# Kernel tuning notes

Hardware: AMD Instinct MI355X
Metric: run time of the kernel (lower is better)

The kernel has to match this reference:

```python
import jax, jax.numpy as jnp
import numpy as np

S, HID, H, D, G = 2048, 4096, 32, 128, 2   # seq, hidden, heads, head_dim, kv groups
ROT = D // 2                               # rotary applied to first half of head_dim
QKV = HID + 2 * G * D                      # 4608


def setup_inputs() -> dict:
    key = jax.random.key(0)
    k1, k2, k3 = jax.random.split(key, 3)
    sc = 0.02
    return {
        "hidden_states": jax.random.normal(k1, (S, HID), jnp.float32),
        "W_qkv": jax.random.normal(k2, (HID, QKV), jnp.float32) * sc,
        "b_qkv": jnp.zeros((QKV,), jnp.float32),
        "W_dense": jax.random.normal(k3, (HID, HID), jnp.float32) * sc,
    }


def _rope(x, pos):
    # x: [S, n_heads, ROT]; interleaved-pair rotation (ChatGLM2 convention)
    half = ROT // 2
    inv_freq = 10000.0 ** (-jnp.arange(0, ROT, 2, dtype=jnp.float32) / ROT)  # [half]
    theta = pos[:, None] * inv_freq                                          # [S, half]
    cos = jnp.cos(theta)[:, None, :]
    sin = jnp.sin(theta)[:, None, :]
    xp = x.reshape(x.shape[0], x.shape[1], half, 2)
    x0, x1 = xp[..., 0], xp[..., 1]
    out = jnp.stack([x0 * cos - x1 * sin, x1 * cos + x0 * sin], axis=-1)
    return out.reshape(x.shape)


def reference(hidden_states, W_qkv, b_qkv, W_dense):
    qkv = hidden_states @ W_qkv + b_qkv            # [S, QKV]
    q = qkv[:, : H * D].reshape(S, H, D)           # [S, H, D]
    k = qkv[:, H * D : H * D + G * D].reshape(S, G, D)
    v = qkv[:, H * D + G * D :].reshape(S, G, D)

    pos = jnp.arange(S, dtype=jnp.float32)
    q = jnp.concatenate([_rope(q[..., :ROT], pos), q[..., ROT:]], axis=-1)
    k = jnp.concatenate([_rope(k[..., :ROT], pos), k[..., ROT:]], axis=-1)

    gidx = jnp.arange(H) % G                       # head -> kv group (MQA/GQA)
    kh = k[:, gidx, :]                             # [S, H, D]
    vh = v[:, gidx, :]

    scores = jnp.einsum('shd,thd->hst', q, kh) / jnp.sqrt(jnp.float32(D))
    causal = jnp.tril(jnp.ones((S, S), bool))
    scores = jnp.where(causal[None], scores, jnp.float32(-1e9))
    p = jax.nn.softmax(scores, axis=-1)            # [H, S, S]
    ctx = jnp.einsum('hst,thd->shd', p, vh).reshape(S, HID)
    return ctx @ W_dense
```

## Files before the change

### kernel.cpp

```cpp
#include <hip/hip_runtime.h>
#include <hip/hip_bf16.h>

#define S_LEN 2048
#define HIDN  4096
#define NH    32
#define HD    128
#define QKV_N 4608
#define K_OFF 4096
#define V_OFF 4352
#define SCALE 0.08838834764831845f

typedef __attribute__((ext_vector_type(8))) short   short8;
typedef __attribute__((ext_vector_type(4))) float   f32x4;
typedef __attribute__((ext_vector_type(4))) unsigned short ushort4v;
typedef __attribute__((ext_vector_type(8))) unsigned short ushort8;

typedef __attribute__((address_space(1))) const unsigned int GU32;
typedef __attribute__((address_space(3))) unsigned int LU32;

__device__ __forceinline__ void async16(const void* g, void* l) {
  __builtin_amdgcn_global_load_lds((GU32*)g, (LU32*)l, 16, 0, 0);
}

__device__ __forceinline__ unsigned short f2bf(float x) {
  __hip_bfloat16 h = __float2bfloat16(x);
  return *reinterpret_cast<unsigned short*>(&h);
}
__device__ __forceinline__ float bf2f(unsigned short u) {
  __hip_bfloat16 h = *reinterpret_cast<__hip_bfloat16*>(&u);
  return __bfloat162float(h);
}

__global__ void k_cvt_bf16(const float* __restrict__ in, unsigned short* __restrict__ out, int n4) {
  int i = blockIdx.x * 256 + threadIdx.x;
  if (i >= n4) return;
  const float4 v = reinterpret_cast<const float4*>(in)[i];
  ushort4v o = { f2bf(v.x), f2bf(v.y), f2bf(v.z), f2bf(v.w) };
  reinterpret_cast<ushort4v*>(out)[i] = o;
}

__global__ __launch_bounds__(256) void k_transpose_cvt(const float* __restrict__ W,
                                                       unsigned short* __restrict__ WT,
                                                       int K, int N) {
  __shared__ float tl[64][65];
  const int n0 = blockIdx.x * 64, k0 = blockIdx.y * 64;
  const int t = threadIdx.x;
  const int r = t >> 4, c4 = (t & 15) << 2;
#pragma unroll
  for (int p = 0; p < 4; ++p) {
    int krow = p * 16 + r;
    const float4 v = *reinterpret_cast<const float4*>(&W[(size_t)(k0 + krow) * N + n0 + c4]);
    tl[krow][c4 + 0] = v.x; tl[krow][c4 + 1] = v.y;
    tl[krow][c4 + 2] = v.z; tl[krow][c4 + 3] = v.w;
  }
  __syncthreads();
#pragma unroll
  for (int p = 0; p < 4; ++p) {
    int nrow = p * 16 + r;
    ushort4v o = { f2bf(tl[c4 + 0][nrow]), f2bf(tl[c4 + 1][nrow]),
                   f2bf(tl[c4 + 2][nrow]), f2bf(tl[c4 + 3][nrow]) };
    *reinterpret_cast<ushort4v*>(&WT[(size_t)(n0 + nrow) * K + k0 + c4]) = o;
  }
}

template <int BIAS, int OUTBF>
__global__ __launch_bounds__(256, 2) void k_gemm_bt(const unsigned short* __restrict__ A,
                                                    const unsigned short* __restrict__ Bt,
                                                    const float* __restrict__ bias,
                                                    void* __restrict__ Cout,
                                                    int M, int N, int K) {
  __shared__ __align__(16) unsigned char lds[32768];
  const int tid = threadIdx.x;
  const int l = tid & 63, w = tid >> 6;
  const int wr = w >> 1, wc = w & 1;
  const int l16 = l & 15, lh = l >> 4;
  const int m0 = blockIdx.y * 128, n0 = blockIdx.x * 128;
  const size_t rowK = (size_t)K * 2;
  const char* Ab = (const char*)A + (size_t)m0 * rowK;
  const char* Bb = (const char*)Bt + (size_t)n0 * rowK;
  f32x4 acc[4][4] = {};
  const int nkt = K >> 6;
  for (int kt = 0; kt < nkt; ++kt) {
    const int kbyte = kt << 7;
#pragma unroll
    for (int rr = 0; rr < 4; ++rr) {
      int off = rr * 4096 + tid * 16;
      int row = off >> 7;
      int col = (off & 127) ^ ((row & 7) << 4);
      async16(Ab + (size_t)row * rowK + kbyte + col, lds + off);
    }
#pragma unroll
    for (int rr = 0; rr < 4; ++rr) {
      int off = rr * 4096 + tid * 16;
      int row = off >> 7;
      int col = (off & 127) ^ ((row & 7) << 4);
      async16(Bb + (size_t)row * rowK + kbyte + col, lds + 16384 + off);
    }
    __syncthreads();
#pragma unroll
    for (int kk = 0; kk < 2; ++kk) {
      short8 af[4], bfr[4];
#pragma unroll
      for (int m = 0; m < 4; ++m) {
        int arow = wr * 64 + m * 16 + l16;
        int byte = (arow << 7) + kk * 64 + lh * 16;
        byte ^= (arow & 7) << 4;
        af[m] = *reinterpret_cast<const short8*>(lds + byte);
      }
#pragma unroll
      for (int n = 0; n < 4; ++n) {
        int brow = wc * 64 + n * 16 + l16;
        int byte = (brow << 7) + kk * 64 + lh * 16;
        byte ^= (brow & 7) << 4;
        bfr[n] = *reinterpret_cast<const short8*>(lds + 16384 + byte);
      }
#pragma unroll
      for (int m = 0; m < 4; ++m)
#pragma unroll
        for (int n = 0; n < 4; ++n)
          acc[m][n] = __builtin_amdgcn_mfma_f32_16x16x32_bf16(af[m], bfr[n], acc[m][n], 0, 0, 0);
    }
    __syncthreads();
  }
#pragma unroll
  for (int m = 0; m < 4; ++m) {
    int grow = m0 + wr * 64 + m * 16 + lh * 4;
#pragma unroll
    for (int n = 0; n < 4; ++n) {
      int gcol = n0 + wc * 64 + n * 16 + l16;
      float bv = BIAS ? bias[gcol] : 0.f;
      f32x4 v = acc[m][n];
#pragma unroll
      for (int j = 0; j < 4; ++j) {
        float val = v[j] + bv;
        if (OUTBF) ((unsigned short*)Cout)[(size_t)(grow + j) * N + gcol] = f2bf(val);
        else       ((float*)Cout)[(size_t)(grow + j) * N + gcol] = val;
      }
    }
  }
}

__global__ void k_rope(unsigned short* __restrict__ qkv) {
  const int p = blockIdx.x * 64 + threadIdx.x;
  const int s = blockIdx.y;
  const int i = p & 31;
  const int hh = p >> 5;
  const int col = (hh < 32) ? (hh * HD + 2 * i) : (K_OFF + (hh - 32) * HD + 2 * i);
  unsigned int* ptr = (unsigned int*)(qkv + (size_t)s * QKV_N + col);
  unsigned int both = *ptr;
  float x0 = bf2f((unsigned short)(both & 0xffffu));
  float x1 = bf2f((unsigned short)(both >> 16));
  float inv = expf(-0.28782313662425572f * (float)i);
  float theta = (float)s * inv;
  float sn, cs;
  sincosf(theta, &sn, &cs);
  float y0 = x0 * cs - x1 * sn;
  float y1 = x1 * cs + x0 * sn;
  *ptr = (unsigned int)f2bf(y0) | ((unsigned int)f2bf(y1) << 16);
}

__global__ __launch_bounds__(256) void k_transpose_v(const unsigned short* __restrict__ qkv,
                                                     unsigned short* __restrict__ Vt) {
  __shared__ __align__(16) unsigned short tl[64][72];
  const int st = blockIdx.x * 64;
  const int dt = blockIdx.y * 64;
  const int g = blockIdx.z;
  const int t = threadIdx.x;
  const int r = t >> 3;
  const int seg = (t & 7) * 8;
#pragma unroll
  for (int p = 0; p < 2; ++p) {
    int srow = p * 32 + r;
    ushort8 v = *reinterpret_cast<const ushort8*>(
        &qkv[(size_t)(st + srow) * QKV_N + V_OFF + g * HD + dt + seg]);
    *reinterpret_cast<ushort8*>(&tl[srow][seg]) = v;
  }
  __syncthreads();
#pragma unroll
  for (int p = 0; p < 2; ++p) {
    int drow = p * 32 + r;
    ushort8 o;
#pragma unroll
    for (int i = 0; i < 8; ++i) o[i] = tl[seg + i][drow];
    *reinterpret_cast<ushort8*>(&Vt[((size_t)g * HD + dt + drow) * S_LEN + st + seg]) = o;
  }
}

__device__ __forceinline__ void stage_kv(const char* Kb, const char* Vb,
                                         unsigned char* ldsK, unsigned char* ldsV, int tid) {
  __builtin_amdgcn_sched_barrier(0);
#pragma unroll
  for (int rr = 0; rr < 4; ++rr) {
    int off = rr * 4096 + tid * 16;
    int row = off >> 8;
    int col = (off & 255) ^ ((row & 7) << 4);
    async16(Kb + (size_t)row * (QKV_N * 2) + col, ldsK + off);
  }
#pragma unroll
  for (int rr = 0; rr < 4; ++rr) {
    int off = rr * 4096 + tid * 16;
    int row = off >> 7;
    int col = (off & 127) ^ ((row & 7) << 4);
    async16(Vb + (size_t)row * (S_LEN * 2) + col, ldsV + off);
  }
  __builtin_amdgcn_sched_barrier(0);
}

__global__ __launch_bounds__(256) void k_attn(const unsigned short* __restrict__ qkv,
                                              const unsigned short* __restrict__ Vt,
                                              unsigned short* __restrict__ ctx) {
  __shared__ __align__(16) unsigned char lds[73728];
  const int tid = threadIdx.x;
  const int l = tid & 63, w = tid >> 6;
  const int l16 = l & 15, lh = l >> 4;
  const int h = blockIdx.y;
  const int g = h & 1;
  const int b = blockIdx.x;
  const int tA = 31 - b;
  const int nA = tA + 1;
  const int nT = nA + b + 1;
  const int q0A = tA * 64, q0B = b * 64;

  const char* Kbase = (const char*)(qkv + K_OFF + g * HD);
  const char* Vbase = (const char*)(Vt + ((size_t)g * HD) * S_LEN);

  short8 vones;
#pragma unroll
  for (int e = 0; e < 8; ++e) vones[e] = (short)0x3F80;

  short8 qf[4];
#pragma unroll
  for (int ks = 0; ks < 4; ++ks)
    qf[ks] = *reinterpret_cast<const short8*>(
        qkv + (size_t)(q0A + w * 16 + l16) * QKV_N + h * HD + ks * 32 + lh * 8);

  f32x4 o[8] = {};
  f32x4 lacc = {};
  float m_run = -1e30f;

  stage_kv(Kbase, Vbase, lds, lds + 32768, tid);

  for (int it = 0; it < nT; ++it) {
    const int phase = (it >= nA) ? 1 : 0;
    const int kt = phase ? (it - nA) : it;
    const int q0 = phase ? q0B : q0A;
    const int k0 = kt << 6;
    const int nxt = it + 1;
    if (nxt < nT) {
      const int kn = ((nxt >= nA) ? (nxt - nA) : nxt) << 6;
      stage_kv(Kbase + (size_t)kn * (QKV_N * 2), Vbase + (size_t)kn * 2,
               lds + (nxt & 1) * 16384, lds + 32768 + (nxt & 1) * 16384, tid);
      asm volatile("s_waitcnt vmcnt(8)" ::: "memory");
    } else {
      asm volatile("s_waitcnt vmcnt(0)" ::: "memory");
    }
    __builtin_amdgcn_s_barrier();
    __builtin_amdgcn_sched_barrier(0);

    const unsigned char* Kl = lds + (it & 1) * 16384;
    const unsigned char* Vl = lds + 32768 + (it & 1) * 16384;

    f32x4 sf[4] = {};
    __builtin_amdgcn_s_setprio(1);
#pragma unroll
    for (int n = 0; n < 4; ++n) {
      int krow = n * 16 + l16;
      int swz = (krow & 7) << 4;
#pragma unroll
      for (int ks = 0; ks < 4; ++ks) {
        int byte = (krow << 8) + ks * 64 + lh * 16;
        short8 kf = *reinterpret_cast<const short8*>(Kl + (byte ^ swz));
        sf[n] = __builtin_amdgcn_mfma_f32_16x16x32_bf16(qf[ks], kf, sf[n], 0, 0, 0);
      }
    }
    __builtin_amdgcn_s_setprio(0);

    const int qrow0 = q0 + w * 16 + lh * 4;
    float tmax = -1e30f;
#pragma unroll
    for (int n = 0; n < 4; ++n) {
      int key = k0 + n * 16 + l16;
#pragma unroll
      for (int j = 0; j < 4; ++j) {
        float v = sf[n][j] * SCALE;
        v = (key <= qrow0 + j) ? v : -1e30f;
        sf[n][j] = v;
        tmax = fmaxf(tmax, v);
      }
    }
#pragma unroll
    for (int d = 1; d < 64; d <<= 1) tmax = fmaxf(tmax, __shfl_xor(tmax, d, 64));
    if (tmax > m_run + 8.f) {
      float fsc = __expf(m_run - tmax);
      m_run = tmax;
#pragma unroll
      for (int n8 = 0; n8 < 8; ++n8) o[n8] *= fsc;
      lacc *= fsc;
    }

    unsigned char* Pb = lds + 65536 + w * 2048;
#pragma unroll
    for (int n = 0; n < 4; ++n)
#pragma unroll
      for (int j = 0; j < 4; ++j) {
        int row = lh * 4 + j;
        int byte = (row << 7) + (n * 16 + l16) * 2;
        byte ^= (row & 7) << 4;
        *(unsigned short*)(Pb + byte) = f2bf(__expf(sf[n][j] - m_run));
      }

    __builtin_amdgcn_s_setprio(1);
#pragma unroll
    for (int kk = 0; kk < 2; ++kk) {
      int pbyte = (l16 << 7) + kk * 64 + lh * 16;
      pbyte ^= (l16 & 7) << 4;
      short8 pa = *reinterpret_cast<const short8*>(Pb + pbyte);
      lacc = __builtin_amdgcn_mfma_f32_16x16x32_bf16(pa, vones, lacc, 0, 0, 0);
#pragma unroll
      for (int n8 = 0; n8 < 8; ++n8) {
        int vrow = n8 * 16 + l16;
        int vbyte = (vrow << 7) + kk * 64 + lh * 16;
        vbyte ^= (vrow & 7) << 4;
        short8 vb = *reinterpret_cast<const short8*>(Vl + vbyte);
        o[n8] = __builtin_amdgcn_mfma_f32_16x16x32_bf16(pa, vb, o[n8], 0, 0, 0);
      }
    }
    __builtin_amdgcn_s_setprio(0);

    if (it == nA - 1) {
#pragma unroll
      for (int n8 = 0; n8 < 8; ++n8) {
        int col = h * HD + n8 * 16 + l16;
#pragma unroll
        for (int j = 0; j < 4; ++j) {
          int row = q0A + w * 16 + lh * 4 + j;
          ctx[(size_t)row * HIDN + col] = f2bf(o[n8][j] / lacc[j]);
        }
      }
#pragma unroll
      for (int n8 = 0; n8 < 8; ++n8) o[n8] = f32x4{0.f, 0.f, 0.f, 0.f};
      lacc = f32x4{0.f, 0.f, 0.f, 0.f};
      m_run = -1e30f;
      __builtin_amdgcn_sched_barrier(0);
#pragma unroll
      for (int ks = 0; ks < 4; ++ks)
        qf[ks] = *reinterpret_cast<const short8*>(
            qkv + (size_t)(q0B + w * 16 + l16) * QKV_N + h * HD + ks * 32 + lh * 8);
      __builtin_amdgcn_sched_barrier(0);
    }
    __builtin_amdgcn_s_barrier();
  }

#pragma unroll
  for (int n8 = 0; n8 < 8; ++n8) {
    int col = h * HD + n8 * 16 + l16;
#pragma unroll
    for (int j = 0; j < 4; ++j) {
      int row = q0B + w * 16 + lh * 4 + j;
      ctx[(size_t)row * HIDN + col] = f2bf(o[n8][j] / lacc[j]);
    }
  }
}

extern "C" void kernel_launch(void* const* d_in, const int* in_sizes, int n_in,
                              void* d_out, int out_size, void* d_ws, size_t ws_size,
                              hipStream_t stream) {
  const float* hidden = (const float*)d_in[0];
  const float* Wqkv = (const float*)d_in[1];
  const float* bqkv = (const float*)d_in[2];
  const float* Wd = (const float*)d_in[3];
  char* ws = (char*)d_ws;
  unsigned short* hid_bf = (unsigned short*)(ws);
  unsigned short* WqkvT  = (unsigned short*)(ws + 16777216);
  unsigned short* WdT    = (unsigned short*)(ws + 54525952);
  unsigned short* qkv    = (unsigned short*)(ws + 88080384);
  unsigned short* Vt     = (unsigned short*)(ws + 106954752);
  unsigned short* ctx    = (unsigned short*)(ws + 108003328);

  k_cvt_bf16<<<8192, 256, 0, stream>>>(hidden, hid_bf, 2097152);
  k_transpose_cvt<<<dim3(72, 64), 256, 0, stream>>>(Wqkv, WqkvT, 4096, 4608);
  k_transpose_cvt<<<dim3(64, 64), 256, 0, stream>>>(Wd, WdT, 4096, 4096);
  k_gemm_bt<1, 1><<<dim3(36, 16), 256, 0, stream>>>(hid_bf, WqkvT, bqkv, qkv, 2048, 4608, 4096);
  k_rope<<<dim3(17, 2048), 64, 0, stream>>>(qkv);
  k_transpose_v<<<dim3(32, 2, 2), 256, 0, stream>>>(qkv, Vt);
  k_attn<<<dim3(16, 32), 256, 0, stream>>>(qkv, Vt, ctx);
  k_gemm_bt<0, 0><<<dim3(32, 16), 256, 0, stream>>>(ctx, WdT, nullptr, d_out, 2048, 4096, 4096);
}
```

Before: 304.3 us.

## Read V directly from global, drop paired causal tiles, raise attention occupancy

The attention kernel stops staging V tiles into LDS and reads V fragments straight from the transposed global buffer, relying on L2/cache hits. It also drops the pairing of a long and a short query tile per block in favour of one query tile per block, with heads on grid x and longest tiles launched first. LDS use falls so that launch bounds can request four blocks per CU. The trade is higher global and L2 traffic and latency on the V reads, plus less even per-block work, in exchange for more resident waves.

```diff
diff --git a/kernel.cpp b/kernel.cpp
--- a/kernel.cpp
+++ b/kernel.cpp
@@ -186,8 +186,7 @@
   }
 }
 
-__device__ __forceinline__ void stage_kv(const char* Kb, const char* Vb,
-                                         unsigned char* ldsK, unsigned char* ldsV, int tid) {
+__device__ __forceinline__ void stage_k(const char* Kb, unsigned char* ldsK, int tid) {
   __builtin_amdgcn_sched_barrier(0);
 #pragma unroll
   for (int rr = 0; rr < 4; ++rr) {
@@ -196,33 +195,23 @@
     int col = (off & 255) ^ ((row & 7) << 4);
     async16(Kb + (size_t)row * (QKV_N * 2) + col, ldsK + off);
   }
-#pragma unroll
-  for (int rr = 0; rr < 4; ++rr) {
-    int off = rr * 4096 + tid * 16;
-    int row = off >> 7;
-    int col = (off & 127) ^ ((row & 7) << 4);
-    async16(Vb + (size_t)row * (S_LEN * 2) + col, ldsV + off);
-  }
   __builtin_amdgcn_sched_barrier(0);
 }
 
-__global__ __launch_bounds__(256) void k_attn(const unsigned short* __restrict__ qkv,
-                                              const unsigned short* __restrict__ Vt,
-                                              unsigned short* __restrict__ ctx) {
-  __shared__ __align__(16) unsigned char lds[73728];
+__global__ __launch_bounds__(256, 4) void k_attn(const unsigned short* __restrict__ qkv,
+                                                 const unsigned short* __restrict__ Vt,
+                                                 unsigned short* __restrict__ ctx) {
+  __shared__ __align__(16) unsigned char lds[40960];
   const int tid = threadIdx.x;
   const int l = tid & 63, w = tid >> 6;
   const int l16 = l & 15, lh = l >> 4;
-  const int h = blockIdx.y;
+  const int h = blockIdx.x;
   const int g = h & 1;
-  const int b = blockIdx.x;
-  const int tA = 31 - b;
-  const int nA = tA + 1;
-  const int nT = nA + b + 1;
-  const int q0A = tA * 64, q0B = b * 64;
+  const int q0 = (31 - blockIdx.y) * 64;
+  const int nkt = (q0 >> 6) + 1;
 
   const char* Kbase = (const char*)(qkv + K_OFF + g * HD);
-  const char* Vbase = (const char*)(Vt + ((size_t)g * HD) * S_LEN);
+  const unsigned short* Vbase = Vt + (size_t)g * HD * S_LEN;
 
   short8 vones;
 #pragma unroll
@@ -232,33 +221,26 @@
 #pragma unroll
   for (int ks = 0; ks < 4; ++ks)
     qf[ks] = *reinterpret_cast<const short8*>(
-        qkv + (size_t)(q0A + w * 16 + l16) * QKV_N + h * HD + ks * 32 + lh * 8);
+        qkv + (size_t)(q0 + w * 16 + l16) * QKV_N + h * HD + ks * 32 + lh * 8);
 
   f32x4 o[8] = {};
   f32x4 lacc = {};
   float m_run = -1e30f;
 
-  stage_kv(Kbase, Vbase, lds, lds + 32768, tid);
-
-  for (int it = 0; it < nT; ++it) {
-    const int phase = (it >= nA) ? 1 : 0;
-    const int kt = phase ? (it - nA) : it;
-    const int q0 = phase ? q0B : q0A;
+  stage_k(Kbase, lds, tid);
+
+  for (int kt = 0; kt < nkt; ++kt) {
     const int k0 = kt << 6;
-    const int nxt = it + 1;
-    if (nxt < nT) {
-      const int kn = ((nxt >= nA) ? (nxt - nA) : nxt) << 6;
-      stage_kv(Kbase + (size_t)kn * (QKV_N * 2), Vbase + (size_t)kn * 2,
-               lds + (nxt & 1) * 16384, lds + 32768 + (nxt & 1) * 16384, tid);
-      asm volatile("s_waitcnt vmcnt(8)" ::: "memory");
+    if (kt + 1 < nkt) {
+      stage_k(Kbase + (size_t)(k0 + 64) * (QKV_N * 2), lds + ((kt + 1) & 1) * 16384, tid);
+      asm volatile("s_waitcnt vmcnt(4)" ::: "memory");
     } else {
       asm volatile("s_waitcnt vmcnt(0)" ::: "memory");
     }
     __builtin_amdgcn_s_barrier();
     __builtin_amdgcn_sched_barrier(0);
 
-    const unsigned char* Kl = lds + (it & 1) * 16384;
-    const unsigned char* Vl = lds + 32768 + (it & 1) * 16384;
+    const unsigned char* Kl = lds + (kt & 1) * 16384;
 
     f32x4 sf[4] = {};
     __builtin_amdgcn_s_setprio(1);
@@ -298,7 +280,7 @@
       lacc *= fsc;
     }
 
-    unsigned char* Pb = lds + 65536 + w * 2048;
+    unsigned char* Pb = lds + 32768 + w * 2048;
 #pragma unroll
     for (int n = 0; n < 4; ++n)
 #pragma unroll
@@ -316,38 +298,22 @@
       pbyte ^= (l16 & 7) << 4;
       short8 pa = *reinterpret_cast<const short8*>(Pb + pbyte);
       lacc = __builtin_amdgcn_mfma_f32_16x16x32_bf16(pa, vones, lacc, 0, 0, 0);
-#pragma unroll
-      for (int n8 = 0; n8 < 8; ++n8) {
-        int vrow = n8 * 16 + l16;
-        int vbyte = (vrow << 7) + kk * 64 + lh * 16;
-        vbyte ^= (vrow & 7) << 4;
-        short8 vb = *reinterpret_cast<const short8*>(Vl + vbyte);
-        o[n8] = __builtin_amdgcn_mfma_f32_16x16x32_bf16(pa, vb, o[n8], 0, 0, 0);
+      const unsigned short* vcol = Vbase + k0 + kk * 32 + lh * 8;
+#pragma unroll
+      for (int half = 0; half < 2; ++half) {
+        short8 vb[4];
+#pragma unroll
+        for (int q = 0; q < 4; ++q) {
+          int n8 = half * 4 + q;
+          vb[q] = *reinterpret_cast<const short8*>(vcol + (size_t)(n8 * 16 + l16) * S_LEN);
+        }
+#pragma unroll
+        for (int q = 0; q < 4; ++q)
+          o[half * 4 + q] = __builtin_amdgcn_mfma_f32_16x16x32_bf16(pa, vb[q], o[half * 4 + q], 0, 0, 0);
       }
     }
     __builtin_amdgcn_s_setprio(0);
 
-    if (it == nA - 1) {
-#pragma unroll
-      for (int n8 = 0; n8 < 8; ++n8) {
-        int col = h * HD + n8 * 16 + l16;
-#pragma unroll
-        for (int j = 0; j < 4; ++j) {
-          int row = q0A + w * 16 + lh * 4 + j;
-          ctx[(size_t)row * HIDN + col] = f2bf(o[n8][j] / lacc[j]);
-        }
-      }
-#pragma unroll
-      for (int n8 = 0; n8 < 8; ++n8) o[n8] = f32x4{0.f, 0.f, 0.f, 0.f};
-      lacc = f32x4{0.f, 0.f, 0.f, 0.f};
-      m_run = -1e30f;
-      __builtin_amdgcn_sched_barrier(0);
-#pragma unroll
-      for (int ks = 0; ks < 4; ++ks)
-        qf[ks] = *reinterpret_cast<const short8*>(
-            qkv + (size_t)(q0B + w * 16 + l16) * QKV_N + h * HD + ks * 32 + lh * 8);
-      __builtin_amdgcn_sched_barrier(0);
-    }
     __builtin_amdgcn_s_barrier();
   }
 
@@ -356,7 +322,7 @@
     int col = h * HD + n8 * 16 + l16;
 #pragma unroll
     for (int j = 0; j < 4; ++j) {
-      int row = q0B + w * 16 + lh * 4 + j;
+      int row = q0 + w * 16 + lh * 4 + j;
       ctx[(size_t)row * HIDN + col] = f2bf(o[n8][j] / lacc[j]);
     }
   }
@@ -383,6 +349,6 @@
   k_gemm_bt<1, 1><<<dim3(36, 16), 256, 0, stream>>>(hid_bf, WqkvT, bqkv, qkv, 2048, 4608, 4096);
   k_rope<<<dim3(17, 2048), 64, 0, stream>>>(qkv);
   k_transpose_v<<<dim3(32, 2, 2), 256, 0, stream>>>(qkv, Vt);
-  k_attn<<<dim3(16, 32), 256, 0, stream>>>(qkv, Vt, ctx);
+  k_attn<<<dim3(32, 32), 256, 0, stream>>>(qkv, Vt, ctx);
   k_gemm_bt<0, 0><<<dim3(32, 16), 256, 0, stream>>>(ctx, WdT, nullptr, d_out, 2048, 4096, 4096);
 }
```

Result: slower. 443.4 us (+45.7%).
